# Performance work log

Measured on AMD Instinct MI355X. Metric: run time of the kernel, lower is better.

Reference implementation:

```python
import jax, jax.numpy as jnp
import numpy as np

# CPC 'same'-mode InfoNCE loss. encoded_x/context: [S, B, L] (steps, batch, latent).
# predictor(context, k) is modeled as a per-k linear map with weight Wk[k] of shape [L, L]
# (y = x @ Wk[k].T), the standard CPC prediction head.

def setup_inputs() -> dict:
    key = jax.random.key(0)
    k1, k2, k3 = jax.random.split(key, 3)
    S, B, L, K = 128, 256, 512, 8
    encoded_x = jax.random.normal(k1, (S, B, L), dtype=jnp.float32)
    context = jax.random.normal(k2, (S, B, L), dtype=jnp.float32)
    Wk = jax.random.normal(k3, (K, L, L), dtype=jnp.float32) * (1.0 / np.sqrt(L))
    return {
        "encoded_x": encoded_x,
        "context": context,
        "Wk": Wk,
        "timesteps_in": 16,
        "timesteps_out": 8,
        "timesteps_ignore": 0,
    }


def reference(encoded_x, context, Wk, timesteps_in, timesteps_out, timesteps_ignore):
    S, B, L = encoded_x.shape
    K = timesteps_out
    # number of inner 'step' iterations: context[T_in : -(K + ignore + 1)]
    steps = S - timesteps_in - (K + timesteps_ignore + 1)
    ctx = context[timesteps_in:timesteps_in + steps]            # [steps, B, L]
    # predictor for all k at once: pred[k, s, b, :] = ctx[s, b] @ Wk[k].T
    pred = jnp.einsum('sbl,kml->ksbm', ctx, Wk)                 # [K, steps, B, L]
    # encoded_latent for each k: encoded_x[T_in + k + 1 : T_in + k + 1 + steps]
    idx = timesteps_in + 1 + jnp.arange(K)[:, None] + jnp.arange(steps)[None, :]
    enc = encoded_x[idx]                                        # [K, steps, B, L]
    # sim[k, s, b, c] = <enc[k,s,b], pred[k,s,c]>  (== mm(enc, pred.T) per (k, step))
    sim = jnp.einsum('ksbl,kscl->ksbc', enc, pred)              # [K, steps, B, B]
    logp = jax.nn.log_softmax(sim, axis=-1)                     # LogSoftmax(dim=-1)
    # loss: sum of diagonals, normalized by -(B * K * steps)
    diag_sum = jnp.einsum('ksbb->', logp)
    denom = B * K * steps
    loss = diag_sum / (-1.0 * denom)
    # correct: argmax over dim 0 (rows, enc axis) per column == arange(B)
    pred_cls = jnp.argmax(logp, axis=2)                         # [K, steps, B]
    correct = jnp.sum(pred_cls == jnp.arange(B)[None, None, :])
    accuracy = correct.astype(jnp.float32) / denom
    return (accuracy, loss)
```

## Files before the change

kernel.cpp:

```cpp
#include <hip/hip_runtime.h>
#include <math.h>
#include <stdint.h>

#define S_DIM 128
#define B_DIM 256
#define L_DIM 512
#define K_DIM 8
#define T_IN  16
#define STEPS 103
#define DENOM (K_DIM * STEPS * B_DIM)
#define PRED_K ((size_t)STEPS * B_DIM * L_DIM)

typedef __attribute__((ext_vector_type(8))) short short8;
typedef __attribute__((ext_vector_type(4))) float f32x4;

__device__ __forceinline__ short f2bf(float f) {
    unsigned u = __float_as_uint(f);
    u += 0x7FFFu + ((u >> 16) & 1u);
    return (short)(u >> 16);
}

__device__ __forceinline__ void load_lds16(const void* g, void* l) {
    __builtin_amdgcn_global_load_lds(
        (const __attribute__((address_space(1))) unsigned*)g,
        (__attribute__((address_space(3))) unsigned*)l, 16, 0, 0);
}

#define ENC4 ((S_DIM * B_DIM * L_DIM) / 4)
#define CTX4 ((STEPS * B_DIM * L_DIM) / 4)
#define WK4  ((K_DIM * L_DIM * L_DIM) / 4)
#define CV_N (ENC4 + CTX4 + WK4)
#define Z_N  (DENOM + 2)
__global__ void convert_all(const float* __restrict__ enc_in, const float* __restrict__ ctx_in,
                            const float* __restrict__ wk_in, short* __restrict__ enc_out,
                            short* __restrict__ ctx_out, short* __restrict__ wk_out,
                            unsigned long long* __restrict__ zbuf) {
    for (int i = blockIdx.x * blockDim.x + threadIdx.x; i < CV_N + Z_N;
         i += gridDim.x * blockDim.x) {
        if (i >= CV_N) { zbuf[i - CV_N] = 0ull; continue; }
        const float4* src; short4* dst; int j;
        if (i < ENC4)             { src = (const float4*)enc_in; dst = (short4*)enc_out; j = i; }
        else if (i < ENC4 + CTX4) { src = (const float4*)ctx_in; dst = (short4*)ctx_out; j = i - ENC4; }
        else                      { src = (const float4*)wk_in;  dst = (short4*)wk_out;  j = i - ENC4 - CTX4; }
        const float4 v = src[j];
        short4 o;
        o.x = f2bf(v.x); o.y = f2bf(v.y); o.z = f2bf(v.z); o.w = f2bf(v.w);
        dst[j] = o;
    }
}

__global__ __launch_bounds__(512, 2)
void gemm_bf16(const short* __restrict__ A, const short* __restrict__ W,
               short* __restrict__ C) {
    __shared__ short As[2][256 * 64];
    __shared__ short Bs[2][256 * 64];
    const int gx  = gridDim.x;
    const int nwg = gx * gridDim.y;
    const int id  = blockIdx.y * gx + blockIdx.x;
    const int q8 = nwg >> 3, r8 = nwg & 7;
    const int xcd = id & 7;
    const int lin = (xcd < r8 ? xcd * (q8 + 1) : r8 * (q8 + 1) + (xcd - r8) * q8)
                  + (id >> 3);
    const int lgx = 31 - __clz(gx);
    const int bm = lin >> lgx;
    const int xc = lin & (gx - 1);
    const int kin = xc >> 1, cn = xc & 1;

    const int t = threadIdx.x;
    const int w = t >> 6, lane = t & 63, quad = lane >> 4, l15 = lane & 15;
    const int wm = w & 3, wn = w >> 2;
    const int rl8 = lane >> 3, ch8 = lane & 7;

    const short* Ab = A + (size_t)bm * 256 * L_DIM;
    const short* Wb = W + ((size_t)kin * L_DIM + cn * 256) * L_DIM;
    short* Ck = C + kin * PRED_K;

    const short* asrc[4]; const short* bsrc[4]; int rdst[4];
    #pragma unroll
    for (int q = 0; q < 4; q++) {
        const int rb = w * 32 + q * 8, row = rb + rl8;
        const int co = (ch8 ^ (row & 7)) * 8;
        asrc[q] = Ab + (size_t)row * L_DIM + co;
        bsrc[q] = Wb + (size_t)row * L_DIM + co;
        rdst[q] = rb * 64;
    }

    #pragma unroll
    for (int q = 0; q < 4; q++) load_lds16(asrc[q], &As[0][rdst[q]]);
    #pragma unroll
    for (int q = 0; q < 4; q++) load_lds16(bsrc[q], &Bs[0][rdst[q]]);
    __syncthreads();

    f32x4 acc[4][8] = {};
    int cur = 0;
    #pragma unroll
    for (int kt = 0; kt < L_DIM; kt += 64) {
        if (kt + 64 < L_DIM) {
            #pragma unroll
            for (int q = 0; q < 4; q++)
                load_lds16(asrc[q] + kt + 64, &As[cur ^ 1][rdst[q]]);
            #pragma unroll
            for (int q = 0; q < 4; q++)
                load_lds16(bsrc[q] + kt + 64, &Bs[cur ^ 1][rdst[q]]);
        }
        #pragma unroll
        for (int k2 = 0; k2 < 2; k2++) {
            short8 a[4], b[8];
            #pragma unroll
            for (int i = 0; i < 4; i++) {
                const int m = wm * 64 + i * 16 + l15;
                a[i] = *(const short8*)&As[cur][m * 64 + ((k2 * 4 + quad) ^ (m & 7)) * 8];
            }
            #pragma unroll
            for (int j = 0; j < 8; j++) {
                const int n = wn * 128 + j * 16 + l15;
                b[j] = *(const short8*)&Bs[cur][n * 64 + ((k2 * 4 + quad) ^ (n & 7)) * 8];
            }
            #pragma unroll
            for (int i = 0; i < 4; i++)
                #pragma unroll
                for (int j = 0; j < 8; j++)
                    acc[i][j] = __builtin_amdgcn_mfma_f32_16x16x32_bf16(a[i], b[j], acc[i][j], 0, 0, 0);
        }
        __syncthreads();
        cur ^= 1;
    }
    #pragma unroll
    for (int i = 0; i < 4; i++)
        #pragma unroll
        for (int r = 0; r < 4; r++) {
            const int row = bm * 256 + wm * 64 + i * 16 + quad * 4 + r;
            short* Cr = Ck + (size_t)row * L_DIM + cn * 256 + wn * 128 + l15;
            #pragma unroll
            for (int j = 0; j < 8; j++)
                Cr[j * 16] = f2bf(acc[i][j][r]);
        }
}

__global__ __launch_bounds__(512, 2)
void sim_phase(const short* __restrict__ encbf, const short* __restrict__ pred,
               const int k0, unsigned long long* __restrict__ col_best,
               float* __restrict__ diag_accum) {
    __shared__ short Es[2][256 * 64];
    __shared__ short Ps[2][256 * 64];
    __shared__ float rmx[256][2];
    __shared__ float rsx[256][2];
    __shared__ float dred[8];
    const int s = blockIdx.x, kin = blockIdx.y;
    const int k = k0 + kin;
    const int t = threadIdx.x, w = t >> 6, lane = t & 63;
    const int quad = lane >> 4, l15 = lane & 15;
    const int wm = w & 3, wn = w >> 2;
    const int rl8 = lane >> 3, ch8 = lane & 7;

    const short* Eb = encbf + ((size_t)(T_IN + 1 + k + s) * B_DIM) * L_DIM;
    const short* Pb = pred + kin * PRED_K + (size_t)s * B_DIM * L_DIM;

    const short* esrc[4]; const short* psrc[4]; int rdst[4];
    #pragma unroll
    for (int q = 0; q < 4; q++) {
        const int rb = w * 32 + q * 8, row = rb + rl8;
        const int co = (ch8 ^ (row & 7)) * 8;
        esrc[q] = Eb + (size_t)row * L_DIM + co;
        psrc[q] = Pb + (size_t)row * L_DIM + co;
        rdst[q] = rb * 64;
    }

    #pragma unroll
    for (int q = 0; q < 4; q++) load_lds16(esrc[q], &Es[0][rdst[q]]);
    #pragma unroll
    for (int q = 0; q < 4; q++) load_lds16(psrc[q], &Ps[0][rdst[q]]);
    __syncthreads();

    f32x4 acc[4][8] = {};
    int cur = 0;
    #pragma unroll
    for (int kt = 0; kt < L_DIM; kt += 64) {
        if (kt + 64 < L_DIM) {
            #pragma unroll
            for (int q = 0; q < 4; q++)
                load_lds16(esrc[q] + kt + 64, &Es[cur ^ 1][rdst[q]]);
            #pragma unroll
            for (int q = 0; q < 4; q++)
                load_lds16(psrc[q] + kt + 64, &Ps[cur ^ 1][rdst[q]]);
        }
        #pragma unroll
        for (int k2 = 0; k2 < 2; k2++) {
            short8 a[4], b[8];
            #pragma unroll
            for (int i = 0; i < 4; i++) {
                const int m = wm * 64 + i * 16 + l15;
                a[i] = *(const short8*)&Es[cur][m * 64 + ((k2 * 4 + quad) ^ (m & 7)) * 8];
            }
            #pragma unroll
            for (int j = 0; j < 8; j++) {
                const int n = wn * 128 + j * 16 + l15;
                b[j] = *(const short8*)&Ps[cur][n * 64 + ((k2 * 4 + quad) ^ (n & 7)) * 8];
            }
            #pragma unroll
            for (int i = 0; i < 4; i++)
                #pragma unroll
                for (int j = 0; j < 8; j++)
                    acc[i][j] = __builtin_amdgcn_mfma_f32_16x16x32_bf16(a[i], b[j], acc[i][j], 0, 0, 0);
        }
        __syncthreads();
        cur ^= 1;
    }

    float rm[4][4];
    #pragma unroll
    for (int i = 0; i < 4; i++)
        #pragma unroll
        for (int r = 0; r < 4; r++) {
            float m = acc[i][0][r];
            #pragma unroll
            for (int j = 1; j < 8; j++) m = fmaxf(m, acc[i][j][r]);
            rm[i][r] = m;
        }
    #pragma unroll
    for (int off = 1; off < 16; off <<= 1)
        #pragma unroll
        for (int i = 0; i < 4; i++)
            #pragma unroll
            for (int r = 0; r < 4; r++)
                rm[i][r] = fmaxf(rm[i][r], __shfl_xor(rm[i][r], off, 64));
    if (l15 == 0)
        #pragma unroll
        for (int i = 0; i < 4; i++)
            #pragma unroll
            for (int r = 0; r < 4; r++)
                rmx[wm * 64 + i * 16 + quad * 4 + r][wn] = rm[i][r];
    __syncthreads();

    float mrow[4][4];
    #pragma unroll
    for (int i = 0; i < 4; i++)
        #pragma unroll
        for (int r = 0; r < 4; r++) {
            const float2 v = *(const float2*)rmx[wm * 64 + i * 16 + quad * 4 + r];
            mrow[i][r] = fmaxf(v.x, v.y);
        }

    float rs[4][4];
    #pragma unroll
    for (int i = 0; i < 4; i++)
        #pragma unroll
        for (int r = 0; r < 4; r++) {
            float sum = 0.f;
            #pragma unroll
            for (int j = 0; j < 8; j++) sum += __expf(acc[i][j][r] - mrow[i][r]);
            rs[i][r] = sum;
        }
    #pragma unroll
    for (int off = 1; off < 16; off <<= 1)
        #pragma unroll
        for (int i = 0; i < 4; i++)
            #pragma unroll
            for (int r = 0; r < 4; r++)
                rs[i][r] += __shfl_xor(rs[i][r], off, 64);
    if (l15 == 0)
        #pragma unroll
        for (int i = 0; i < 4; i++)
            #pragma unroll
            for (int r = 0; r < 4; r++)
                rsx[wm * 64 + i * 16 + quad * 4 + r][wn] = rs[i][r];
    __syncthreads();

    float lse[4][4];
    #pragma unroll
    for (int i = 0; i < 4; i++)
        #pragma unroll
        for (int r = 0; r < 4; r++) {
            const float2 v = *(const float2*)rsx[wm * 64 + i * 16 + quad * 4 + r];
            lse[i][r] = mrow[i][r] + __logf(v.x + v.y);
        }

    #pragma unroll
    for (int j = 0; j < 8; j++) {
        unsigned long long best = 0;
        #pragma unroll
        for (int i = 0; i < 4; i++)
            #pragma unroll
            for (int r = 0; r < 4; r++) {
                const int grow = wm * 64 + i * 16 + quad * 4 + r;
                const float v = acc[i][j][r] - lse[i][r];
                unsigned int fb = __float_as_uint(v);
                fb = (fb & 0x80000000u) ? ~fb : (fb | 0x80000000u);
                const unsigned long long p =
                    ((unsigned long long)fb << 32) | (unsigned long long)(255 - grow);
                if (p > best) best = p;
            }
        unsigned long long o;
        o = __shfl_xor(best, 16, 64); if (o > best) best = o;
        o = __shfl_xor(best, 32, 64); if (o > best) best = o;
        if (quad == 0)
            atomicMax(&col_best[((size_t)k * STEPS + s) * B_DIM + wn * 128 + j * 16 + l15], best);
    }

    {
        float dv = 0.f;
        #pragma unroll
        for (int i = 0; i < 4; i++)
            #pragma unroll
            for (int j = 0; j < 8; j++)
                #pragma unroll
                for (int r = 0; r < 4; r++) {
                    const int grow = wm * 64 + i * 16 + quad * 4 + r;
                    const int c = wn * 128 + j * 16 + l15;
                    if (grow == c) dv += acc[i][j][r] - lse[i][r];
                }
        #pragma unroll
        for (int off = 1; off < 64; off <<= 1) dv += __shfl_xor(dv, off, 64);
        if (lane == 0) dred[w] = dv;
    }
    __syncthreads();
    if (t == 0) {
        float dv = 0.f;
        #pragma unroll
        for (int i = 0; i < 8; i++) dv += dred[i];
        atomicAdd(diag_accum, dv);
    }
}

__global__ void count_finalize(const unsigned long long* __restrict__ col_best,
                               int* __restrict__ correct_accum,
                               float* __restrict__ diag_accum,
                               unsigned int* __restrict__ done,
                               float* __restrict__ out) {
    __shared__ int red[256];
    const int t = threadIdx.x;
    int cnt = 0;
    for (int i = blockIdx.x * 256 + t; i < DENOM; i += gridDim.x * 256) {
        const int c = i & (B_DIM - 1);
        const int b = 255 - (int)(col_best[i] & 0xFFFFFFFFull);
        cnt += (b == c) ? 1 : 0;
    }
    red[t] = cnt;
    __syncthreads();
    for (int off = 128; off > 0; off >>= 1) {
        if (t < off) red[t] += red[t + off];
        __syncthreads();
    }
    if (t == 0) {
        atomicAdd(correct_accum, red[0]);
        __threadfence();
        if (atomicAdd(done, 1u) == gridDim.x - 1) {
            const int   c = atomicAdd(correct_accum, 0);
            const float d = atomicAdd(diag_accum, 0.0f);
            const float denom = (float)DENOM;
            out[0] = (float)c / denom;
            out[1] = -d / denom;
        }
    }
}

extern "C" void kernel_launch(void* const* d_in, const int* in_sizes, int n_in,
                              void* d_out, int out_size, void* d_ws, size_t ws_size,
                              hipStream_t stream) {
    const float* encoded_x = (const float*)d_in[0];
    const float* context   = (const float*)d_in[1];
    const float* Wk        = (const float*)d_in[2];
    float* out = (float*)d_out;

    const size_t enc_elems = (size_t)S_DIM * B_DIM * L_DIM;
    const size_t ctx_elems = (size_t)STEPS * B_DIM * L_DIM;
    const size_t wk_elems  = (size_t)K_DIM * L_DIM * L_DIM;
    const size_t pred_k_bytes = ctx_elems * 2;

    char* ws = (char*)d_ws;
    short* encbf = (short*)ws;
    short* ctxbf = (short*)(ws + enc_elems * 2);
    short* wkbf  = (short*)(ws + (enc_elems + ctx_elems) * 2);
    const size_t off = (enc_elems + ctx_elems + wk_elems) * 2;
    unsigned long long* col_best = (unsigned long long*)(ws + off);
    float* diag_accum    = (float*)(ws + off + (size_t)DENOM * 8);
    int*   correct_accum = (int*)  (ws + off + (size_t)DENOM * 8 + 4);
    unsigned int* done   = (unsigned int*)(ws + off + (size_t)DENOM * 8 + 8);
    const size_t fixed = off + (size_t)DENOM * 8 + 64;
    short* pred = (short*)(ws + fixed);

    int g = K_DIM;
    while (g > 1 && fixed + (size_t)g * pred_k_bytes > ws_size) g >>= 1;

    convert_all<<<2048, 256, 0, stream>>>(encoded_x, context + (size_t)T_IN * B_DIM * L_DIM,
                                          Wk, encbf, ctxbf, wkbf, col_best);

    const dim3 g1(2 * g, 103);
    const dim3 g2(STEPS, g);
    for (int k0 = 0; k0 < K_DIM; k0 += g) {
        gemm_bf16<<<g1, 512, 0, stream>>>(ctxbf, wkbf + (size_t)k0 * L_DIM * L_DIM, pred);
        sim_phase<<<g2, 512, 0, stream>>>(encbf, pred, k0, col_best, diag_accum);
    }
    count_finalize<<<64, 256, 0, stream>>>(col_best, correct_accum, diag_accum, done, out);
}
```

Baseline: 431.3 us.

## Replace double-buffered LDS pipeline with single-buffer load-sync-compute loop in both GEMMs

Both the projection GEMM and the similarity kernel drop the two-stage LDS ping-pong buffers. Each K-tile is now loaded, synchronised and consumed before the next one is fetched. This halves LDS use per block, which could allow more resident blocks per CU, and removes the prologue and buffer-index bookkeeping. In exchange, global-to-LDS loads no longer overlap with MFMA work inside a block, so latency hiding depends entirely on occupancy.

```diff
diff --git a/kernel.cpp b/kernel.cpp
--- a/kernel.cpp
+++ b/kernel.cpp
@@ -52,8 +52,8 @@
 __global__ __launch_bounds__(512, 2)
 void gemm_bf16(const short* __restrict__ A, const short* __restrict__ W,
                short* __restrict__ C) {
-    __shared__ short As[2][256 * 64];
-    __shared__ short Bs[2][256 * 64];
+    __shared__ short As[256 * 64];
+    __shared__ short Bs[256 * 64];
     const int gx  = gridDim.x;
     const int nwg = gx * gridDim.y;
     const int id  = blockIdx.y * gx + blockIdx.x;
@@ -85,36 +85,25 @@
         rdst[q] = rb * 64;
     }
 
-    #pragma unroll
-    for (int q = 0; q < 4; q++) load_lds16(asrc[q], &As[0][rdst[q]]);
-    #pragma unroll
-    for (int q = 0; q < 4; q++) load_lds16(bsrc[q], &Bs[0][rdst[q]]);
-    __syncthreads();
-
     f32x4 acc[4][8] = {};
-    int cur = 0;
-    #pragma unroll
     for (int kt = 0; kt < L_DIM; kt += 64) {
-        if (kt + 64 < L_DIM) {
-            #pragma unroll
-            for (int q = 0; q < 4; q++)
-                load_lds16(asrc[q] + kt + 64, &As[cur ^ 1][rdst[q]]);
-            #pragma unroll
-            for (int q = 0; q < 4; q++)
-                load_lds16(bsrc[q] + kt + 64, &Bs[cur ^ 1][rdst[q]]);
-        }
+        #pragma unroll
+        for (int q = 0; q < 4; q++) load_lds16(asrc[q] + kt, &As[rdst[q]]);
+        #pragma unroll
+        for (int q = 0; q < 4; q++) load_lds16(bsrc[q] + kt, &Bs[rdst[q]]);
+        __syncthreads();
         #pragma unroll
         for (int k2 = 0; k2 < 2; k2++) {
             short8 a[4], b[8];
             #pragma unroll
             for (int i = 0; i < 4; i++) {
                 const int m = wm * 64 + i * 16 + l15;
-                a[i] = *(const short8*)&As[cur][m * 64 + ((k2 * 4 + quad) ^ (m & 7)) * 8];
+                a[i] = *(const short8*)&As[m * 64 + ((k2 * 4 + quad) ^ (m & 7)) * 8];
             }
             #pragma unroll
             for (int j = 0; j < 8; j++) {
                 const int n = wn * 128 + j * 16 + l15;
-                b[j] = *(const short8*)&Bs[cur][n * 64 + ((k2 * 4 + quad) ^ (n & 7)) * 8];
+                b[j] = *(const short8*)&Bs[n * 64 + ((k2 * 4 + quad) ^ (n & 7)) * 8];
             }
             #pragma unroll
             for (int i = 0; i < 4; i++)
@@ -123,7 +112,6 @@
                     acc[i][j] = __builtin_amdgcn_mfma_f32_16x16x32_bf16(a[i], b[j], acc[i][j], 0, 0, 0);
         }
         __syncthreads();
-        cur ^= 1;
     }
     #pragma unroll
     for (int i = 0; i < 4; i++)
@@ -141,8 +129,8 @@
 void sim_phase(const short* __restrict__ encbf, const short* __restrict__ pred,
                const int k0, unsigned long long* __restrict__ col_best,
                float* __restrict__ diag_accum) {
-    __shared__ short Es[2][256 * 64];
-    __shared__ short Ps[2][256 * 64];
+    __shared__ short Es[256 * 64];
+    __shared__ short Ps[256 * 64];
     __shared__ float rmx[256][2];
     __shared__ float rsx[256][2];
     __shared__ float dred[8];
@@ -166,36 +154,25 @@
         rdst[q] = rb * 64;
     }
 
-    #pragma unroll
-    for (int q = 0; q < 4; q++) load_lds16(esrc[q], &Es[0][rdst[q]]);
-    #pragma unroll
-    for (int q = 0; q < 4; q++) load_lds16(psrc[q], &Ps[0][rdst[q]]);
-    __syncthreads();
-
     f32x4 acc[4][8] = {};
-    int cur = 0;
-    #pragma unroll
     for (int kt = 0; kt < L_DIM; kt += 64) {
-        if (kt + 64 < L_DIM) {
-            #pragma unroll
-            for (int q = 0; q < 4; q++)
-                load_lds16(esrc[q] + kt + 64, &Es[cur ^ 1][rdst[q]]);
-            #pragma unroll
-            for (int q = 0; q < 4; q++)
-                load_lds16(psrc[q] + kt + 64, &Ps[cur ^ 1][rdst[q]]);
-        }
+        #pragma unroll
+        for (int q = 0; q < 4; q++) load_lds16(esrc[q] + kt, &Es[rdst[q]]);
+        #pragma unroll
+        for (int q = 0; q < 4; q++) load_lds16(psrc[q] + kt, &Ps[rdst[q]]);
+        __syncthreads();
         #pragma unroll
         for (int k2 = 0; k2 < 2; k2++) {
             short8 a[4], b[8];
             #pragma unroll
             for (int i = 0; i < 4; i++) {
                 const int m = wm * 64 + i * 16 + l15;
-                a[i] = *(const short8*)&Es[cur][m * 64 + ((k2 * 4 + quad) ^ (m & 7)) * 8];
+                a[i] = *(const short8*)&Es[m * 64 + ((k2 * 4 + quad) ^ (m & 7)) * 8];
             }
             #pragma unroll
             for (int j = 0; j < 8; j++) {
                 const int n = wn * 128 + j * 16 + l15;
-                b[j] = *(const short8*)&Ps[cur][n * 64 + ((k2 * 4 + quad) ^ (n & 7)) * 8];
+                b[j] = *(const short8*)&Ps[n * 64 + ((k2 * 4 + quad) ^ (n & 7)) * 8];
             }
             #pragma unroll
             for (int i = 0; i < 4; i++)
@@ -204,7 +181,6 @@
                     acc[i][j] = __builtin_amdgcn_mfma_f32_16x16x32_bf16(a[i], b[j], acc[i][j], 0, 0, 0);
         }
         __syncthreads();
-        cur ^= 1;
     }
 
     float rm[4][4];
```

Result: slower. 462.8 us (+7.3%).
